# Kernel optimization log

Measured on AMD Instinct MI355X. Metric: run time of the kernel, lower is better.

Reference implementation:

```python
import jax, jax.numpy as jnp
import numpy as np

N_LAYERS = 8
N_MODELS = 9  # 1 big + 8 lil
F = 512
SPLIT = 16384
N_LIL = 2048  # rows per lil model; lil rows total = (N_MODELS-1)*N_LIL = 16384


def setup_inputs() -> dict:
    key = jax.random.key(0)
    k_x, k_wb, k_bb, k_wl, k_bl = jax.random.split(key, 5)
    scale = 1.0 / np.sqrt(F)  # keep activations stable across 8 layers
    x = jax.random.normal(k_x, (SPLIT + (N_MODELS - 1) * N_LIL, F), dtype=jnp.float32)
    Wbig = jax.random.normal(k_wb, (N_LAYERS, F, F), dtype=jnp.float32) * scale
    Bbig = jax.random.normal(k_bb, (N_LAYERS, F), dtype=jnp.float32) * 0.01
    Wlil = jax.random.normal(k_wl, (N_LAYERS, N_MODELS - 1, F, F), dtype=jnp.float32) * scale
    Blil = jax.random.normal(k_bl, (N_LAYERS, N_MODELS - 1, F), dtype=jnp.float32) * 0.01
    return {"x": x, "Wbig": Wbig, "Bbig": Bbig, "Wlil": Wlil, "Blil": Blil,
            "split": SPLIT, "n_lil": N_LIL}


def reference(x, Wbig, Bbig, Wlil, Blil, split, n_lil):
    n_layers, f = Wbig.shape[0], x.shape[1]
    n_lil_models = Wlil.shape[1]

    # Big stream: addmm(B, y, W) == y @ W + B, per layer.
    ybig = x[:split]
    for l in range(n_layers):
        ybig = ybig @ Wbig[l] + Bbig[l]

    # Lil stream: rows are grouped in blocks of n_lil per lil model
    # (repeat_interleave semantics). baddbmm(B[...,None], W, y[...,None])
    # computes (W @ y) + B per row => y @ W[m].T within model m.
    ylil = x[split:].reshape(n_lil_models, n_lil, f)  # [m, n, f]
    for l in range(n_layers):
        ylil = jnp.einsum('mnf,mgf->mng', ylil, Wlil[l]) + Blil[l][:, None, :]

    return jnp.concatenate([ybig, ylil.reshape(-1, f)], axis=0)
```

## Files before the change

kernel.cpp:

```cpp
#include <hip/hip_runtime.h>

typedef __bf16 bf16_t;
typedef bf16_t bf16x8 __attribute__((ext_vector_type(8)));
typedef bf16_t bf16x4 __attribute__((ext_vector_type(4)));
typedef float f32x4 __attribute__((ext_vector_type(4)));

#define F 512
#define NLAYERS 8
#define NLIL 8
#define TM 128

__global__ void transpose_wbig(const float* __restrict__ W, bf16_t* __restrict__ out) {
  __shared__ float tile[64][65];
  const int l = blockIdx.z;
  const int tf = blockIdx.x, tg = blockIdx.y;
  const float* Wl = W + (size_t)l * F * F;
  bf16_t* Ol = out + (size_t)l * F * F;
  const int tx = threadIdx.x & 63;
  const int ty = threadIdx.x >> 6;
#pragma unroll
  for (int i = 0; i < 16; ++i) {
    int f = i * 4 + ty;
    tile[f][tx] = Wl[(size_t)(tf * 64 + f) * F + tg * 64 + tx];
  }
  __syncthreads();
#pragma unroll
  for (int i = 0; i < 16; ++i) {
    int g = i * 4 + ty;
    Ol[(size_t)(tg * 64 + g) * F + tf * 64 + tx] = (bf16_t)tile[tx][g];
  }
}

__global__ void convert_w(const float4* __restrict__ in, bf16x4* __restrict__ out, int n4) {
  int stride = gridDim.x * blockDim.x;
  for (int i = blockIdx.x * blockDim.x + threadIdx.x; i < n4; i += stride) {
    float4 v = in[i];
    bf16x4 o;
    o[0] = (bf16_t)v.x; o[1] = (bf16_t)v.y; o[2] = (bf16_t)v.z; o[3] = (bf16_t)v.w;
    out[i] = o;
  }
}

__device__ __forceinline__ int ysw(int m, int k) {
  return m * F + ((((k >> 3) ^ (m & 7)) << 3) | (k & 7));
}

template <bool PREP>
__global__ __launch_bounds__(1024, 4) void fused_mlp(
    const float* __restrict__ x,
    const bf16_t* __restrict__ WbigT, const bf16_t* __restrict__ WlilT,
    const float* __restrict__ WbigF, const float* __restrict__ WlilF,
    const float* __restrict__ Bbig, const float* __restrict__ Blil,
    float* __restrict__ out) {
  __shared__ alignas(16) bf16_t Y[TM * F];

  const int tid = threadIdx.x;
  const int lane = tid & 63;
  const int wave = tid >> 6;
  const int ln15 = lane & 15;
  const int q = lane >> 4;
  const int kq = q << 3;
  const int rq = q << 2;
  const int g0 = wave * 32;

  const int bid = blockIdx.x;
  const int xcd = bid & 7;
  const int slot = bid >> 3;
  int model, rb;
  if (slot < 16) { model = 1 + xcd; rb = slot; }
  else           { model = 0; rb = (xcd << 4) + (slot - 16); }

  const size_t grow = (model == 0) ? (size_t)rb * TM
                                   : (size_t)(16384 + (model - 1) * 2048 + rb * TM);

  {
    const float4* xs = (const float4*)(x + grow * F);
#pragma unroll
    for (int i = 0; i < 16; ++i) {
      int f4 = tid + i * 1024;
      int row = f4 >> 7;
      int c4 = f4 & 127;
      float4 v = xs[f4];
      bf16x4 o;
      o[0] = (bf16_t)v.x; o[1] = (bf16_t)v.y; o[2] = (bf16_t)v.z; o[3] = (bf16_t)v.w;
      *(bf16x4*)&Y[ysw(row, c4 * 4)] = o;
    }
  }
  __syncthreads();

  for (int l = 0; l < NLAYERS; ++l) {
    const bf16_t* Wt = nullptr;
    const float* Wf = nullptr;
    if (PREP)
      Wt = (model == 0) ? WbigT + (size_t)l * F * F
                        : WlilT + (size_t)(l * NLIL + (model - 1)) * F * F;
    else
      Wf = (model == 0) ? WbigF + (size_t)l * F * F
                        : WlilF + (size_t)(l * NLIL + (model - 1)) * F * F;
    const float* Bp = (model == 0) ? Bbig + (size_t)l * F
                                   : Blil + (size_t)(l * NLIL + (model - 1)) * F;

    f32x4 acc[2][8];
#pragma unroll
    for (int gi = 0; gi < 2; ++gi) {
      f32x4 bi = *(const f32x4*)&Bp[g0 + gi * 16 + rq];
#pragma unroll
      for (int mi = 0; mi < 8; ++mi) acc[gi][mi] = bi;
    }

#pragma unroll 2
    for (int ks = 0; ks < 16; ++ks) {
      const int kk = ks * 32 + kq;
      bf16x8 aW[2];
      if (PREP) {
#pragma unroll
        for (int gi = 0; gi < 2; ++gi)
          aW[gi] = *(const bf16x8*)&Wt[(size_t)(g0 + gi * 16 + ln15) * F + kk];
      } else if (model != 0) {
#pragma unroll
        for (int gi = 0; gi < 2; ++gi) {
          const float* p = Wf + (size_t)(g0 + gi * 16 + ln15) * F + kk;
          float4 u = *(const float4*)p;
          float4 v = *(const float4*)(p + 4);
          bf16x8 t;
          t[0] = (bf16_t)u.x; t[1] = (bf16_t)u.y; t[2] = (bf16_t)u.z; t[3] = (bf16_t)u.w;
          t[4] = (bf16_t)v.x; t[5] = (bf16_t)v.y; t[6] = (bf16_t)v.z; t[7] = (bf16_t)v.w;
          aW[gi] = t;
        }
      } else {
#pragma unroll
        for (int gi = 0; gi < 2; ++gi) {
          int col = g0 + gi * 16 + ln15;
          bf16x8 t;
#pragma unroll
          for (int j = 0; j < 8; ++j) t[j] = (bf16_t)Wf[(size_t)(kk + j) * F + col];
          aW[gi] = t;
        }
      }
      bf16x8 bY[8];
      const int chunk = (ks * 4 + q) ^ (ln15 & 7);
#pragma unroll
      for (int mi = 0; mi < 8; ++mi)
        bY[mi] = *(const bf16x8*)&Y[(mi * 16 + ln15) * F + (chunk << 3)];
#pragma unroll
      for (int gi = 0; gi < 2; ++gi)
#pragma unroll
        for (int mi = 0; mi < 8; ++mi)
          acc[gi][mi] = __builtin_amdgcn_mfma_f32_16x16x32_bf16(aW[gi], bY[mi], acc[gi][mi], 0, 0, 0);
    }
    __syncthreads();

    if (l < NLAYERS - 1) {
#pragma unroll
      for (int gi = 0; gi < 2; ++gi)
#pragma unroll
        for (int mi = 0; mi < 8; ++mi) {
          int m = mi * 16 + ln15;
          int g = g0 + gi * 16 + rq;
          bf16x4 t;
#pragma unroll
          for (int r = 0; r < 4; ++r) t[r] = (bf16_t)acc[gi][mi][r];
          *(bf16x4*)&Y[ysw(m, g)] = t;
        }
      __syncthreads();
    } else {
      float* op = out + grow * F;
#pragma unroll
      for (int gi = 0; gi < 2; ++gi)
#pragma unroll
        for (int mi = 0; mi < 8; ++mi) {
          int m = mi * 16 + ln15;
          int g = g0 + gi * 16 + rq;
          *(f32x4*)&op[(size_t)m * F + g] = acc[gi][mi];
        }
    }
  }
}

extern "C" void kernel_launch(void* const* d_in, const int* in_sizes, int n_in,
                              void* d_out, int out_size, void* d_ws, size_t ws_size,
                              hipStream_t stream) {
  const float* x    = (const float*)d_in[0];
  const float* Wbig = (const float*)d_in[1];
  const float* Bbig = (const float*)d_in[2];
  const float* Wlil = (const float*)d_in[3];
  const float* Blil = (const float*)d_in[4];
  float* out = (float*)d_out;

  const size_t nWbig = (size_t)NLAYERS * F * F;
  const size_t nWlil = (size_t)NLAYERS * NLIL * F * F;
  const size_t need = (nWbig + nWlil) * sizeof(bf16_t);

  if (ws_size >= need) {
    bf16_t* WbigT = (bf16_t*)d_ws;
    bf16_t* WlilB = WbigT + nWbig;
    transpose_wbig<<<dim3(8, 8, NLAYERS), 256, 0, stream>>>(Wbig, WbigT);
    convert_w<<<4096, 256, 0, stream>>>((const float4*)Wlil, (bf16x4*)WlilB,
                                        (int)(nWlil / 4));
    fused_mlp<true><<<256, 1024, 0, stream>>>(x, WbigT, WlilB, nullptr, nullptr,
                                              Bbig, Blil, out);
  } else {
    fused_mlp<false><<<256, 1024, 0, stream>>>(x, nullptr, nullptr, Wbig, Wlil,
                                               Bbig, Blil, out);
  }
}
```

Before: 329.7 us.

## Retile waves to 64x64 output tiles and merge weight prep kernels

Each wave now computes a 64-column by 64-row output tile (4x4 MFMA fragments) instead of 32 columns by all 128 rows (2x8). This balances weight and activation fragment loads per MFMA, cutting shared-memory Y reads, while doubling the global weight fragments each wave loads per k-step. The two weight preparation kernels (big transpose and lil conversion) are also merged into one launch, removing one kernel launch and letting both run concurrently.

```diff
diff --git a/kernel.cpp b/kernel.cpp
--- a/kernel.cpp
+++ b/kernel.cpp
@@ -10,34 +10,37 @@
 #define NLIL 8
 #define TM 128
 
-__global__ void transpose_wbig(const float* __restrict__ W, bf16_t* __restrict__ out) {
-  __shared__ float tile[64][65];
-  const int l = blockIdx.z;
-  const int tf = blockIdx.x, tg = blockIdx.y;
-  const float* Wl = W + (size_t)l * F * F;
-  bf16_t* Ol = out + (size_t)l * F * F;
-  const int tx = threadIdx.x & 63;
-  const int ty = threadIdx.x >> 6;
-#pragma unroll
-  for (int i = 0; i < 16; ++i) {
-    int f = i * 4 + ty;
-    tile[f][tx] = Wl[(size_t)(tf * 64 + f) * F + tg * 64 + tx];
-  }
-  __syncthreads();
-#pragma unroll
-  for (int i = 0; i < 16; ++i) {
-    int g = i * 4 + ty;
-    Ol[(size_t)(tg * 64 + g) * F + tf * 64 + tx] = (bf16_t)tile[tx][g];
-  }
-}
-
-__global__ void convert_w(const float4* __restrict__ in, bf16x4* __restrict__ out, int n4) {
-  int stride = gridDim.x * blockDim.x;
-  for (int i = blockIdx.x * blockDim.x + threadIdx.x; i < n4; i += stride) {
-    float4 v = in[i];
-    bf16x4 o;
-    o[0] = (bf16_t)v.x; o[1] = (bf16_t)v.y; o[2] = (bf16_t)v.z; o[3] = (bf16_t)v.w;
-    out[i] = o;
+__global__ void prep_weights(const float* __restrict__ Wbig, bf16_t* __restrict__ WbigT,
+                             const float4* __restrict__ Wlil, bf16x4* __restrict__ WlilB,
+                             int n4) {
+  if (blockIdx.x < 512) {
+    __shared__ float tile[64][65];
+    const int b = blockIdx.x;
+    const int l = b >> 6;
+    const int tf = (b >> 3) & 7, tg = b & 7;
+    const float* Wl = Wbig + (size_t)l * F * F;
+    bf16_t* Ol = WbigT + (size_t)l * F * F;
+    const int tx = threadIdx.x & 63;
+    const int ty = threadIdx.x >> 6;
+#pragma unroll
+    for (int i = 0; i < 16; ++i) {
+      int f = i * 4 + ty;
+      tile[f][tx] = Wl[(size_t)(tf * 64 + f) * F + tg * 64 + tx];
+    }
+    __syncthreads();
+#pragma unroll
+    for (int i = 0; i < 16; ++i) {
+      int g = i * 4 + ty;
+      Ol[(size_t)(tg * 64 + g) * F + tf * 64 + tx] = (bf16_t)tile[tx][g];
+    }
+  } else {
+    const int stride = (gridDim.x - 512) * blockDim.x;
+    for (int i = (blockIdx.x - 512) * blockDim.x + threadIdx.x; i < n4; i += stride) {
+      float4 v = Wlil[i];
+      bf16x4 o;
+      o[0] = (bf16_t)v.x; o[1] = (bf16_t)v.y; o[2] = (bf16_t)v.z; o[3] = (bf16_t)v.w;
+      WlilB[i] = o;
+    }
   }
 }
 
@@ -61,7 +64,10 @@
   const int q = lane >> 4;
   const int kq = q << 3;
   const int rq = q << 2;
-  const int g0 = wave * 32;
+  const int gs = wave & 7;
+  const int mh = wave >> 3;
+  const int g0 = gs * 64;
+  const int m0 = mh * 64;
 
   const int bid = blockIdx.x;
   const int xcd = bid & 7;
@@ -100,25 +106,25 @@
     const float* Bp = (model == 0) ? Bbig + (size_t)l * F
                                    : Blil + (size_t)(l * NLIL + (model - 1)) * F;
 
-    f32x4 acc[2][8];
-#pragma unroll
-    for (int gi = 0; gi < 2; ++gi) {
+    f32x4 acc[4][4];
+#pragma unroll
+    for (int gi = 0; gi < 4; ++gi) {
       f32x4 bi = *(const f32x4*)&Bp[g0 + gi * 16 + rq];
 #pragma unroll
-      for (int mi = 0; mi < 8; ++mi) acc[gi][mi] = bi;
+      for (int mi = 0; mi < 4; ++mi) acc[gi][mi] = bi;
     }
 
 #pragma unroll 2
     for (int ks = 0; ks < 16; ++ks) {
       const int kk = ks * 32 + kq;
-      bf16x8 aW[2];
+      bf16x8 aW[4];
       if (PREP) {
 #pragma unroll
-        for (int gi = 0; gi < 2; ++gi)
+        for (int gi = 0; gi < 4; ++gi)
           aW[gi] = *(const bf16x8*)&Wt[(size_t)(g0 + gi * 16 + ln15) * F + kk];
       } else if (model != 0) {
 #pragma unroll
-        for (int gi = 0; gi < 2; ++gi) {
+        for (int gi = 0; gi < 4; ++gi) {
           const float* p = Wf + (size_t)(g0 + gi * 16 + ln15) * F + kk;
           float4 u = *(const float4*)p;
           float4 v = *(const float4*)(p + 4);
@@ -129,7 +135,7 @@
         }
       } else {
 #pragma unroll
-        for (int gi = 0; gi < 2; ++gi) {
+        for (int gi = 0; gi < 4; ++gi) {
           int col = g0 + gi * 16 + ln15;
           bf16x8 t;
 #pragma unroll
@@ -137,25 +143,25 @@
           aW[gi] = t;
         }
       }
-      bf16x8 bY[8];
+      bf16x8 bY[4];
       const int chunk = (ks * 4 + q) ^ (ln15 & 7);
 #pragma unroll
-      for (int mi = 0; mi < 8; ++mi)
-        bY[mi] = *(const bf16x8*)&Y[(mi * 16 + ln15) * F + (chunk << 3)];
-#pragma unroll
-      for (int gi = 0; gi < 2; ++gi)
-#pragma unroll
-        for (int mi = 0; mi < 8; ++mi)
+      for (int mi = 0; mi < 4; ++mi)
+        bY[mi] = *(const bf16x8*)&Y[(m0 + mi * 16 + ln15) * F + (chunk << 3)];
+#pragma unroll
+      for (int gi = 0; gi < 4; ++gi)
+#pragma unroll
+        for (int mi = 0; mi < 4; ++mi)
           acc[gi][mi] = __builtin_amdgcn_mfma_f32_16x16x32_bf16(aW[gi], bY[mi], acc[gi][mi], 0, 0, 0);
     }
     __syncthreads();
 
     if (l < NLAYERS - 1) {
 #pragma unroll
-      for (int gi = 0; gi < 2; ++gi)
-#pragma unroll
-        for (int mi = 0; mi < 8; ++mi) {
-          int m = mi * 16 + ln15;
+      for (int gi = 0; gi < 4; ++gi)
+#pragma unroll
+        for (int mi = 0; mi < 4; ++mi) {
+          int m = m0 + mi * 16 + ln15;
           int g = g0 + gi * 16 + rq;
           bf16x4 t;
 #pragma unroll
@@ -166,10 +172,10 @@
     } else {
       float* op = out + grow * F;
 #pragma unroll
-      for (int gi = 0; gi < 2; ++gi)
-#pragma unroll
-        for (int mi = 0; mi < 8; ++mi) {
-          int m = mi * 16 + ln15;
+      for (int gi = 0; gi < 4; ++gi)
+#pragma unroll
+        for (int mi = 0; mi < 4; ++mi) {
+          int m = m0 + mi * 16 + ln15;
           int g = g0 + gi * 16 + rq;
           *(f32x4*)&op[(size_t)m * F + g] = acc[gi][mi];
         }
@@ -194,9 +200,8 @@
   if (ws_size >= need) {
     bf16_t* WbigT = (bf16_t*)d_ws;
     bf16_t* WlilB = WbigT + nWbig;
-    transpose_wbig<<<dim3(8, 8, NLAYERS), 256, 0, stream>>>(Wbig, WbigT);
-    convert_w<<<4096, 256, 0, stream>>>((const float4*)Wlil, (bf16x4*)WlilB,
-                                        (int)(nWlil / 4));
+    prep_weights<<<4608, 256, 0, stream>>>(Wbig, WbigT, (const float4*)Wlil,
+                                           (bf16x4*)WlilB, (int)(nWlil / 4));
     fused_mlp<true><<<256, 1024, 0, stream>>>(x, WbigT, WlilB, nullptr, nullptr,
                                               Bbig, Blil, out);
   } else {
```

New measurement: 441.0 us. 1.34x slower.
